# Kernel optimization log

Hardware: AMD Instinct MI355X
Metric: run time of the kernel (lower is better)

Reference implementation:

```python
import jax, jax.numpy as jnp
import numpy as np

N = 50000      # nodes
E = 800000     # edges
H = 128        # hidden_features
DEPTH = 5
G = 64         # graphs in batch
EPS = 1e-5


def _ln(x, g, b):
    m = jnp.mean(x, axis=-1, keepdims=True)
    v = jnp.mean((x - m) ** 2, axis=-1, keepdims=True)
    return (x - m) * jax.lax.rsqrt(v + EPS) * g + b


def _lin_init(key, fan_in, fan_out):
    s = 1.0 / np.sqrt(fan_in)
    kw, kb = jax.random.split(key)
    return (jax.random.uniform(kw, (fan_in, fan_out), jnp.float32, -s, s),
            jax.random.uniform(kb, (fan_out,), jnp.float32, -s, s))


def setup_inputs() -> dict:
    key = jax.random.key(0)
    ks = jax.random.split(key, 16)
    inp = {
        'x': jax.random.normal(ks[0], (N, 1), jnp.float32),
        'pos': jax.random.normal(ks[1], (N, 3), jnp.float32),
        'edge_index': jax.random.randint(ks[2], (2, E), 0, N, jnp.int32),
        'cell_offset': jax.random.normal(ks[3], (E, 3), jnp.float32),
        'unit_cell': jax.random.normal(ks[4], (3, 3), jnp.float32),
        'batch_ids': jnp.sort(jax.random.randint(ks[5], (N,), 0, G, jnp.int32)),
    }
    inp['emb_w'], inp['emb_b'] = _lin_init(ks[6], 1, H)
    # stacked per-layer params for lax.scan
    def stack(fn):
        outs = [fn(jax.random.fold_in(ks[7], i)) for i in range(DEPTH)]
        return tuple(jnp.stack(t) for t in zip(*outs))
    def layer_params(k):
        k1, k2, k3, k4 = jax.random.split(k, 4)
        mw1, mb1 = _lin_init(k1, 2 * H + 1, H)
        mw2, mb2 = _lin_init(k2, H, H)
        uw1, ub1 = _lin_init(k3, 2 * H, H)
        uw2, ub2 = _lin_init(k4, H, H)
        ones = jnp.ones((H,), jnp.float32); zeros = jnp.zeros((H,), jnp.float32)
        return (mw1, mb1, ones, zeros, mw2, mb2, ones, zeros,
                uw1, ub1, ones, zeros, uw2, ub2, ones, zeros)
    (inp['msg_w1'], inp['msg_b1'], inp['msg_g1'], inp['msg_be1'],
     inp['msg_w2'], inp['msg_b2'], inp['msg_g2'], inp['msg_be2'],
     inp['upd_w1'], inp['upd_b1'], inp['upd_g1'], inp['upd_be1'],
     inp['upd_w2'], inp['upd_b2'], inp['upd_g2'], inp['upd_be2']) = stack(layer_params)
    inp['pred_w1'], inp['pred_b1'] = _lin_init(ks[8], H, H)
    inp['pred_w2'], inp['pred_b2'] = _lin_init(ks[9], H, 1)
    return inp


def reference(x, pos, edge_index, cell_offset, unit_cell, batch_ids,
              emb_w, emb_b,
              msg_w1, msg_b1, msg_g1, msg_be1, msg_w2, msg_b2, msg_g2, msg_be2,
              upd_w1, upd_b1, upd_g1, upd_be1, upd_w2, upd_b2, upd_g2, upd_be2,
              pred_w1, pred_b1, pred_w2, pred_b2):
    src, dst = edge_index[0], edge_index[1]  # PyG: x_j = source, x_i = target
    h = x @ emb_w + emb_b  # [N, H]
    # PBC distances
    corrected = pos[dst] - cell_offset @ unit_cell  # [E, 3]
    dist = jnp.linalg.norm(corrected - pos[src], axis=-1, keepdims=True)  # [E, 1]

    def step(h, p):
        (mw1, mb1, mg1, mbe1, mw2, mb2, mg2, mbe2,
         uw1, ub1, ug1, ube1, uw2, ub2, ug2, ube2) = p
        msg = jnp.concatenate([h[dst], h[src], dist], axis=-1)  # [E, 2H+1]
        msg = jax.nn.relu(_ln(msg @ mw1 + mb1, mg1, mbe1))
        msg = jax.nn.relu(_ln(msg @ mw2 + mb2, mg2, mbe2))
        aggr = jax.ops.segment_sum(msg, dst, num_segments=N)  # scatter-add to targets
        u = jnp.concatenate([h, aggr], axis=-1)  # [N, 2H]
        u = jax.nn.relu(_ln(u @ uw1 + ub1, ug1, ube1))
        u = jax.nn.relu(_ln(u @ uw2 + ub2, ug2, ube2))
        return h + u, None  # residual

    params = (msg_w1, msg_b1, msg_g1, msg_be1, msg_w2, msg_b2, msg_g2, msg_be2,
              upd_w1, upd_b1, upd_g1, upd_be1, upd_w2, upd_b2, upd_g2, upd_be2)
    h, _ = jax.lax.scan(step, h, params)
    pooled = jax.ops.segment_sum(h, batch_ids, num_segments=G)  # global_add_pool
    return jax.nn.relu(pooled @ pred_w1 + pred_b1) @ pred_w2 + pred_b2  # [G, 1]
```

## Files before the change

### kernel.cpp

```cpp
#include <hip/hip_runtime.h>
#include <hip/hip_bf16.h>

#define NN 50000
#define NE 800000
#define HD 128
#define DEPTH 5
#define NG 64
#define LNEPS 1e-5f

typedef __attribute__((ext_vector_type(8))) short bf8;
typedef __attribute__((ext_vector_type(4))) float f4;

static __device__ __forceinline__ unsigned short bf1(float x) {
    __hip_bfloat16 b = __float2bfloat16(x);
    unsigned short r;
    __builtin_memcpy(&r, &b, 2);
    return r;
}
static __device__ __forceinline__ unsigned int cvt2(float a, float b) {
    float2 t; t.x = a; t.y = b;
    __hip_bfloat162 h = __float22bfloat162_rn(t);
    unsigned int r;
    __builtin_memcpy(&r, &h, 4);
    return r;
}


__global__ void pack_weights(const float* __restrict__ msg_w1, const float* __restrict__ msg_w2,
                             const float* __restrict__ upd_w1, const float* __restrict__ upd_w2,
                             unsigned short* __restrict__ packed) {
    const int which = blockIdx.y & 3, layer = blockIdx.y >> 2;
    const int t = blockIdx.x * 256 + threadIdx.x;
    unsigned short* lbase = packed + layer * 98304;
    if (which == 0) {
        if (t >= 32768) return;
        const int e = t & 7, l = (t >> 3) & 63, f = (t >> 9) & 15, s = t >> 13;
        const int k = s*32 + ((l >> 4) << 3) + e;
        const float* W = msg_w1 + layer*257*HD;
        const float v = (f < 8) ? W[k*HD + f*16 + (l & 15)]
                                : W[(k + 128)*HD + (f - 8)*16 + (l & 15)];
        lbase[t] = bf1(v);
        return;
    }
    const float* src; int K; unsigned short* dst;
    if (which == 1)      { src = msg_w2 + layer*HD*HD;  K = 128; dst = lbase + 32768; }
    else if (which == 2) { src = upd_w1 + layer*256*HD; K = 256; dst = lbase + 49152; }
    else                 { src = upd_w2 + layer*HD*HD;  K = 128; dst = lbase + 81920; }
    if (t >= K * HD) return;
    const int e = t & 7, l = (t >> 3) & 63, f = (t >> 9) & 7, s = t >> 12;
    const int kk = s*32 + ((l >> 4) << 3) + e;
    const int k = (which & 1) ? ((kk & 7)*16 + (kk >> 3)) : kk;
    const int n = f*16 + (l & 15);
    dst[t] = bf1(src[k*HD + n]);
}

__global__ void pack_sig(const float* __restrict__ msg_w1, const float* __restrict__ msg_g1,
                         const float* __restrict__ msg_be1, float* __restrict__ sig) {
    const int t = blockIdx.x * 256 + threadIdx.x;
    if (t >= DEPTH * 384) return;
    const int layer = t / 384, w3 = (t % 384) / 128, i = t % 128;
    const int col = (i & 7)*16 + (i >> 3);
    float v;
    if (w3 == 0)      v = msg_w1[layer*257*HD + 256*HD + col];
    else if (w3 == 1) v = msg_g1[layer*HD + col];
    else              v = msg_be1[layer*HD + col];
    sig[t] = v;
}

__global__ void embed_kernel(const float* __restrict__ x, const float* __restrict__ emb_w,
                             const float* __restrict__ emb_b,
                             float* __restrict__ h, unsigned short* __restrict__ hb) {
    const int i = blockIdx.x * 256 + threadIdx.x;
    const int n = i >> 7, j = i & 127;
    const float v = x[n] * emb_w[j] + emb_b[j];
    h[i] = v; hb[i] = bf1(v);
}

__global__ void hist_kernel(const int* __restrict__ ei, int* __restrict__ cnt) {
    const int e = blockIdx.x * 256 + threadIdx.x;
    atomicAdd(&cnt[ei[NE + e]], 1);
}

__global__ __launch_bounds__(1024) void scan_kernel(const int* __restrict__ cnt,
                                                    int* __restrict__ cur) {
    __shared__ int part[1024];
    const int t = threadIdx.x;
    const int per = 49;
    const int base = t * per;
    int s = 0;
    for (int i = 0; i < per; ++i) { const int idx = base + i; if (idx < NN) s += cnt[idx]; }
    part[t] = s; __syncthreads();
    for (int st = 1; st < 1024; st <<= 1) {
        const int v = (t >= st) ? part[t - st] : 0;
        __syncthreads();
        part[t] += v;
        __syncthreads();
    }
    int run = (t == 0) ? 0 : part[t - 1];
    for (int i = 0; i < per; ++i) {
        const int idx = base + i;
        if (idx < NN) { cur[idx] = run; run += cnt[idx]; }
    }
}

__global__ void scatter_kernel(const int* __restrict__ ei, int* __restrict__ cur,
                               int* __restrict__ sidx, int* __restrict__ ssrc,
                               int* __restrict__ sdst) {
    const int e = blockIdx.x * 256 + threadIdx.x;
    const int d = ei[NE + e];
    const int p = atomicAdd(&cur[d], 1);
    sidx[p] = e; ssrc[p] = ei[e]; sdst[p] = d;
}

__global__ void dist_kernel(const float* __restrict__ pos, const int* __restrict__ sidx,
                            const int* __restrict__ ssrc, const int* __restrict__ sdst,
                            const float* __restrict__ cell, const float* __restrict__ U,
                            float* __restrict__ dist) {
    const int p = blockIdx.x * 256 + threadIdx.x;
    const int e = sidx[p];
    const int s = ssrc[p], d = sdst[p];
    const float c0 = cell[e*3], c1 = cell[e*3+1], c2 = cell[e*3+2];
    const float ox = c0*U[0] + c1*U[3] + c2*U[6];
    const float oy = c0*U[1] + c1*U[4] + c2*U[7];
    const float oz = c0*U[2] + c1*U[5] + c2*U[8];
    const float dx = pos[d*3]   - ox - pos[s*3];
    const float dy = pos[d*3+1] - oy - pos[s*3+1];
    const float dz = pos[d*3+2] - oz - pos[s*3+2];
    dist[p] = sqrtf(dx*dx + dy*dy + dz*dz);
}

__global__ __launch_bounds__(256, 4) void y_kernel(const unsigned short* __restrict__ hb,
                         const unsigned short* __restrict__ pw,
                         const float* __restrict__ b1, unsigned short* __restrict__ y) {
    const int tid = threadIdx.x, blk = blockIdx.x;
    const int l = tid & 63, wv = tid >> 6;
    const int li = l & 15, gq = l >> 4;
    const int row = wv*16 + li;
    const int node0 = blk*64 + row;
    const int nc = (node0 < NN) ? node0 : NN - 1;
    const unsigned short* pH = hb + nc*HD + gq*8;

    f4 acc[16];
    #pragma unroll
    for (int f = 0; f < 16; ++f) { f4 z = {0.f,0.f,0.f,0.f}; acc[f] = z; }

    #pragma unroll
    for (int s = 0; s < 4; ++s) {
        const bf8 a = *(const bf8*)(pH + s*32);
        #pragma unroll
        for (int f = 0; f < 16; ++f) {
            const bf8 b = *(const bf8*)(pw + s*8192 + f*512 + l*8);
            acc[f] = __builtin_amdgcn_mfma_f32_16x16x32_bf16(a, b, acc[f], 0, 0, 0);
        }
    }

    float bv[8];
    #pragma unroll
    for (int f = 0; f < 8; ++f) bv[f] = b1[f*16 + li];

    #pragma unroll
    for (int r = 0; r < 4; ++r) {
        const int node = blk*64 + wv*16 + gq*4 + r;
        if (node < NN) {
            uint4 u;
            u.x = cvt2(acc[0][r]+bv[0], acc[1][r]+bv[1]);
            u.y = cvt2(acc[2][r]+bv[2], acc[3][r]+bv[3]);
            u.z = cvt2(acc[4][r]+bv[4], acc[5][r]+bv[5]);
            u.w = cvt2(acc[6][r]+bv[6], acc[7][r]+bv[7]);
            *(uint4*)(y + node*256 + li*8) = u;
            uint4 v;
            v.x = cvt2(acc[8][r],  acc[9][r]);
            v.y = cvt2(acc[10][r], acc[11][r]);
            v.z = cvt2(acc[12][r], acc[13][r]);
            v.w = cvt2(acc[14][r], acc[15][r]);
            *(uint4*)(y + node*256 + 128 + li*8) = v;
        }
    }
}

__global__ __launch_bounds__(128, 4) void edge_kernel(
    const unsigned short* __restrict__ y, const float* __restrict__ dist,
    const int* __restrict__ ssrc, const int* __restrict__ sdst,
    const unsigned short* __restrict__ pw2, const float* __restrict__ sig,
    const float* __restrict__ b2, const float* __restrict__ g2,
    const float* __restrict__ be2, float* __restrict__ aggr)
{
    __shared__ unsigned short lds[64 * 128];
    __shared__ int dstl[64];
    char* ldsb = (char*)lds;
    const int tid = threadIdx.x, blk = blockIdx.x;
    const int l = tid & 63, wv = tid >> 6;
    const int li = l & 15, gq = l >> 4;

    if (tid < 64) dstl[tid] = sdst[blk*64 + tid];

    {
        const int rl = l >> 1, half = l & 1;
        const int row = wv*32 + rl;
        const int e = blk*64 + row;
        const int dn = sdst[e], sn = ssrc[e];
        const float dv = dist[e];
        const unsigned short* pd = y + dn*256 + half*64;
        const unsigned short* pS = y + sn*256 + 128 + half*64;
        const float* wl = sig + half*64;

        float msum[64];
        #pragma unroll
        for (int c = 0; c < 8; ++c) {
            const uint4 ud = *(const uint4*)(pd + c*8);
            const uint4 us = *(const uint4*)(pS + c*8);
            const float4 wa = *(const float4*)(wl + c*8);
            const float4 wb = *(const float4*)(wl + c*8 + 4);
            const unsigned int du[4] = {ud.x, ud.y, ud.z, ud.w};
            const unsigned int su[4] = {us.x, us.y, us.z, us.w};
            const float ww[8] = {wa.x,wa.y,wa.z,wa.w, wb.x,wb.y,wb.z,wb.w};
            #pragma unroll
            for (int k = 0; k < 4; ++k) {
                const float d0 = __uint_as_float(du[k] << 16);
                const float d1 = __uint_as_float(du[k] & 0xffff0000u);
                const float s0 = __uint_as_float(su[k] << 16);
                const float s1 = __uint_as_float(su[k] & 0xffff0000u);
                msum[c*8 + 2*k]     = d0 + s0 + dv*ww[2*k];
                msum[c*8 + 2*k + 1] = d1 + s1 + dv*ww[2*k+1];
            }
        }
        float s1 = 0.f, s2 = 0.f;
        #pragma unroll
        for (int i = 0; i < 64; ++i) { s1 += msum[i]; s2 += msum[i]*msum[i]; }
        s1 += __shfl_xor(s1, 1);
        s2 += __shfl_xor(s2, 1);
        const float mean = s1 * (1.f/HD);
        const float rstd = rsqrtf(s2*(1.f/HD) - mean*mean + LNEPS);

        const float* g1p = sig + 128 + half*64;
        const float* e1p = sig + 256 + half*64;
        const int rsw = (row & 15) << 4;
        const int base = row*256 + half*128;
        #pragma unroll
        for (int c = 0; c < 8; ++c) {
            const float4 ga = *(const float4*)(g1p + c*8);
            const float4 gb = *(const float4*)(g1p + c*8 + 4);
            const float4 ea = *(const float4*)(e1p + c*8);
            const float4 eb = *(const float4*)(e1p + c*8 + 4);
            const float gg[8] = {ga.x,ga.y,ga.z,ga.w, gb.x,gb.y,gb.z,gb.w};
            const float ee[8] = {ea.x,ea.y,ea.z,ea.w, eb.x,eb.y,eb.z,eb.w};
            float t[8];
            #pragma unroll
            for (int k = 0; k < 8; ++k)
                t[k] = fmaxf((msum[c*8+k] - mean)*rstd*gg[k] + ee[k], 0.f);
            uint4 u;
            u.x = cvt2(t[0], t[1]); u.y = cvt2(t[2], t[3]);
            u.z = cvt2(t[4], t[5]); u.w = cvt2(t[6], t[7]);
            *(uint4*)(ldsb + ((base + c*16) ^ rsw)) = u;
        }
    }

    f4 acc2[2][8];
    #pragma unroll
    for (int m = 0; m < 2; ++m)
        #pragma unroll
        for (int f = 0; f < 8; ++f) { f4 z = {0.f,0.f,0.f,0.f}; acc2[m][f] = z; }
    #pragma unroll
    for (int s = 0; s < 4; ++s) {
        bf8 breg[8];
        #pragma unroll
        for (int f = 0; f < 8; ++f) breg[f] = *(const bf8*)(pw2 + s*4096 + f*512 + l*8);
        #pragma unroll
        for (int m = 0; m < 2; ++m) {
            const int ar = wv*32 + m*16 + li;
            const bf8 a = *(const bf8*)(ldsb + ((ar*256 + s*64 + gq*16) ^ ((ar & 15) << 4)));
            #pragma unroll
            for (int f = 0; f < 8; ++f)
                acc2[m][f] = __builtin_amdgcn_mfma_f32_16x16x32_bf16(a, breg[f], acc2[m][f], 0, 0, 0);
        }
    }

    {
        float bb2[8], gg2[8], be2v[8];
        #pragma unroll
        for (int f = 0; f < 8; ++f) {
            const int n = f*16 + li;
            bb2[f] = b2[n]; gg2[f] = g2[n]; be2v[f] = be2[n];
        }
        #pragma unroll
        for (int m = 0; m < 2; ++m) {
            float ps[4] = {0,0,0,0}, pq[4] = {0,0,0,0};
            #pragma unroll
            for (int f = 0; f < 8; ++f)
                #pragma unroll
                for (int r = 0; r < 4; ++r) {
                    const float v = acc2[m][f][r] + bb2[f];
                    acc2[m][f][r] = v;
                    ps[r] += v; pq[r] += v*v;
                }
            #pragma unroll
            for (int mm = 1; mm < 16; mm <<= 1)
                #pragma unroll
                for (int r = 0; r < 4; ++r) {
                    ps[r] += __shfl_xor(ps[r], mm);
                    pq[r] += __shfl_xor(pq[r], mm);
                }
            #pragma unroll
            for (int r = 0; r < 4; ++r) {
                const float mean = ps[r] * (1.f/HD);
                const float rstd = rsqrtf(pq[r]*(1.f/HD) - mean*mean + LNEPS);
                const int row = wv*32 + m*16 + gq*4 + r;
                float vv[8];
                #pragma unroll
                for (int f = 0; f < 8; ++f)
                    vv[f] = fmaxf((acc2[m][f][r] - mean)*rstd*gg2[f] + be2v[f], 0.f);
                uint4 u;
                u.x = cvt2(vv[0], vv[1]); u.y = cvt2(vv[2], vv[3]);
                u.z = cvt2(vv[4], vv[5]); u.w = cvt2(vv[6], vv[7]);
                *(uint4*)(ldsb + ((row*256 + li*16) ^ ((row & 15) << 4))) = u;
            }
        }
    }
    __syncthreads();

    {
        const int jp = tid & 63, hh = tid >> 6;
        const int j0 = jp*2, j1 = j0 + 1;
        const int jj0 = (j0 & 7)*16 + (j0 >> 3);
        const int jj1 = (j1 & 7)*16 + (j1 >> 3);
        const int r0 = hh * 32;
        int curd = dstl[r0];
        float a0 = 0.f, a1 = 0.f;
        #pragma unroll 4
        for (int i = 0; i < 32; ++i) {
            const int row = r0 + i;
            const int d = dstl[row];
            const unsigned int u = *(const unsigned int*)(ldsb + ((row*256 + jp*4) ^ ((row & 15) << 4)));
            if (d != curd) {
                unsafeAtomicAdd(&aggr[curd*HD + jj0], a0);
                unsafeAtomicAdd(&aggr[curd*HD + jj1], a1);
                a0 = a1 = 0.f; curd = d;
            }
            a0 += __uint_as_float(u << 16);
            a1 += __uint_as_float(u & 0xffff0000u);
        }
        unsafeAtomicAdd(&aggr[curd*HD + jj0], a0);
        unsafeAtomicAdd(&aggr[curd*HD + jj1], a1);
    }
}

__global__ __launch_bounds__(256, 4) void node_kernel(
    unsigned short* __restrict__ hb, float* __restrict__ aggr,
    const unsigned short* __restrict__ pw,
    const float* __restrict__ b1, const float* __restrict__ g1, const float* __restrict__ be1,
    const float* __restrict__ b2, const float* __restrict__ g2, const float* __restrict__ be2,
    float* __restrict__ h)
{
    __shared__ unsigned short lds[64 * 128];
    char* ldsb = (char*)lds;
    const int tid = threadIdx.x, blk = blockIdx.x;
    const int l = tid & 63, wv = tid >> 6;
    const int li = l & 15, gq = l >> 4;

    const int row = wv*16 + li;
    const int nA = blk*64 + row;
    const int nc = (nA < NN) ? nA : NN - 1;
    const unsigned short* pH = hb + nc*HD + gq*8;
    float* pA = aggr + nc*HD + gq*8;

    f4 acc[8];
    #pragma unroll
    for (int f = 0; f < 8; ++f) { f4 z = {0.f,0.f,0.f,0.f}; acc[f] = z; }

    #pragma unroll
    for (int s = 0; s < 8; ++s) {
        bf8 breg[8];
        #pragma unroll
        for (int f = 0; f < 8; ++f) breg[f] = *(const bf8*)(pw + s*4096 + f*512 + l*8);
        bf8 a;
        if (s < 4) {
            a = *(const bf8*)(pH + s*32);
        } else {
            const float4 a0 = *(const float4*)(pA + (s-4)*32);
            const float4 a1 = *(const float4*)(pA + (s-4)*32 + 4);
            union { unsigned int u[4]; bf8 v; } pk;
            pk.u[0] = cvt2(a0.x, a0.y); pk.u[1] = cvt2(a0.z, a0.w);
            pk.u[2] = cvt2(a1.x, a1.y); pk.u[3] = cvt2(a1.z, a1.w);
            a = pk.v;
        }
        #pragma unroll
        for (int f = 0; f < 8; ++f)
            acc[f] = __builtin_amdgcn_mfma_f32_16x16x32_bf16(a, breg[f], acc[f], 0, 0, 0);
    }

    {
        const float4 z = {0.f,0.f,0.f,0.f};
        if (nA < NN) {
            #pragma unroll
            for (int s = 0; s < 4; ++s) { *(float4*)(pA + s*32) = z; *(float4*)(pA + s*32 + 4) = z; }
        }
    }

    {
        float bb[8], gg[8], be[8];
        #pragma unroll
        for (int f = 0; f < 8; ++f) {
            const int n = f*16 + li;
            bb[f] = b1[n]; gg[f] = g1[n]; be[f] = be1[n];
        }
        float ps[4] = {0,0,0,0}, pq[4] = {0,0,0,0};
        #pragma unroll
        for (int f = 0; f < 8; ++f)
            #pragma unroll
            for (int r = 0; r < 4; ++r) {
                const float v = acc[f][r] + bb[f];
                acc[f][r] = v;
                ps[r] += v; pq[r] += v*v;
            }
        #pragma unroll
        for (int mm = 1; mm < 16; mm <<= 1)
            #pragma unroll
            for (int r = 0; r < 4; ++r) {
                ps[r] += __shfl_xor(ps[r], mm);
                pq[r] += __shfl_xor(pq[r], mm);
            }
        #pragma unroll
        for (int r = 0; r < 4; ++r) {
            const float mean = ps[r] * (1.f/HD);
            const float rstd = rsqrtf(pq[r]*(1.f/HD) - mean*mean + LNEPS);
            const int rw = wv*16 + gq*4 + r;
            float vv[8];
            #pragma unroll
            for (int f = 0; f < 8; ++f)
                vv[f] = fmaxf((acc[f][r] - mean)*rstd*gg[f] + be[f], 0.f);
            uint4 u;
            u.x = cvt2(vv[0], vv[1]); u.y = cvt2(vv[2], vv[3]);
            u.z = cvt2(vv[4], vv[5]); u.w = cvt2(vv[6], vv[7]);
            *(uint4*)(ldsb + ((rw*256 + li*16) ^ ((rw & 15) << 4))) = u;
        }
    }

    const unsigned short* pw2 = pw + 32768;
    f4 acc2[8];
    #pragma unroll
    for (int f = 0; f < 8; ++f) { f4 z = {0.f,0.f,0.f,0.f}; acc2[f] = z; }
    #pragma unroll
    for (int s = 0; s < 4; ++s) {
        bf8 breg[8];
        #pragma unroll
        for (int f = 0; f < 8; ++f) breg[f] = *(const bf8*)(pw2 + s*4096 + f*512 + l*8);
        const int ar = wv*16 + li;
        const bf8 a = *(const bf8*)(ldsb + ((ar*256 + s*64 + gq*16) ^ ((ar & 15) << 4)));
        #pragma unroll
        for (int f = 0; f < 8; ++f)
            acc2[f] = __builtin_amdgcn_mfma_f32_16x16x32_bf16(a, breg[f], acc2[f], 0, 0, 0);
    }

    {
        float bb2[8], gg2[8], be2v[8];
        #pragma unroll
        for (int f = 0; f < 8; ++f) {
            const int n = f*16 + li;
            bb2[f] = b2[n]; gg2[f] = g2[n]; be2v[f] = be2[n];
        }
        float ps[4] = {0,0,0,0}, pq[4] = {0,0,0,0};
        #pragma unroll
        for (int f = 0; f < 8; ++f)
            #pragma unroll
            for (int r = 0; r < 4; ++r) {
                const float v = acc2[f][r] + bb2[f];
                acc2[f][r] = v;
                ps[r] += v; pq[r] += v*v;
            }
        #pragma unroll
        for (int mm = 1; mm < 16; mm <<= 1)
            #pragma unroll
            for (int r = 0; r < 4; ++r) {
                ps[r] += __shfl_xor(ps[r], mm);
                pq[r] += __shfl_xor(pq[r], mm);
            }
        #pragma unroll
        for (int r = 0; r < 4; ++r) {
            const int node = blk*64 + wv*16 + gq*4 + r;
            if (node < NN) {
                const float mean = ps[r] * (1.f/HD);
                const float rstd = rsqrtf(pq[r]*(1.f/HD) - mean*mean + LNEPS);
                #pragma unroll
                for (int f = 0; f < 8; ++f) {
                    const int n = f*16 + li;
                    float v = (acc2[f][r] - mean)*rstd*gg2[f] + be2v[f];
                    v = fmaxf(v, 0.f);
                    const int idx = node*HD + n;
                    const float nh = h[idx] + v;
                    h[idx] = nh;
                    hb[idx] = bf1(nh);
                }
            }
        }
    }
}

__global__ void pool_kernel(const float* __restrict__ h, const int* __restrict__ bids,
                            float* __restrict__ pooled) {
    const int j = threadIdx.x;
    const int n0 = blockIdx.x * 256;
    if (n0 >= NN) return;
    int cur = bids[n0];
    float acc = 0.f;
    for (int i = 0; i < 256; ++i) {
        const int n = n0 + i;
        if (n >= NN) break;
        const int b = bids[n];
        if (b != cur) { unsafeAtomicAdd(&pooled[cur*HD + j], acc); acc = 0.f; cur = b; }
        acc += h[n*HD + j];
    }
    unsafeAtomicAdd(&pooled[cur*HD + j], acc);
}

__global__ void pred_kernel(const float* __restrict__ pooled, const float* __restrict__ w1,
                            const float* __restrict__ pb1, const float* __restrict__ w2,
                            const float* __restrict__ pb2, float* __restrict__ out) {
    const int g = blockIdx.x, j = threadIdx.x;
    __shared__ float pg[128];
    __shared__ float red[128];
    pg[j] = pooled[g*HD + j];
    __syncthreads();
    float z = pb1[j];
    for (int k = 0; k < 128; ++k) z += pg[k] * w1[k*HD + j];
    red[j] = fmaxf(z, 0.f) * w2[j];
    __syncthreads();
    for (int st = 64; st > 0; st >>= 1) {
        if (j < st) red[j] += red[j + st];
        __syncthreads();
    }
    if (j == 0) out[g] = red[0] + pb2[0];
}

extern "C" void kernel_launch(void* const* d_in, const int* in_sizes, int n_in,
                              void* d_out, int out_size, void* d_ws, size_t ws_size,
                              hipStream_t stream) {
    const float* x       = (const float*)d_in[0];
    const float* pos     = (const float*)d_in[1];
    const int*   ei      = (const int*)  d_in[2];
    const float* cell    = (const float*)d_in[3];
    const float* U       = (const float*)d_in[4];
    const int*   bids    = (const int*)  d_in[5];
    const float* emb_w   = (const float*)d_in[6];
    const float* emb_b   = (const float*)d_in[7];
    const float* msg_w1  = (const float*)d_in[8];
    const float* msg_b1  = (const float*)d_in[9];
    const float* msg_g1  = (const float*)d_in[10];
    const float* msg_be1 = (const float*)d_in[11];
    const float* msg_w2  = (const float*)d_in[12];
    const float* msg_b2  = (const float*)d_in[13];
    const float* msg_g2  = (const float*)d_in[14];
    const float* msg_be2 = (const float*)d_in[15];
    const float* upd_w1  = (const float*)d_in[16];
    const float* upd_b1  = (const float*)d_in[17];
    const float* upd_g1  = (const float*)d_in[18];
    const float* upd_be1 = (const float*)d_in[19];
    const float* upd_w2  = (const float*)d_in[20];
    const float* upd_b2  = (const float*)d_in[21];
    const float* upd_g2  = (const float*)d_in[22];
    const float* upd_be2 = (const float*)d_in[23];
    const float* pred_w1 = (const float*)d_in[24];
    const float* pred_b1 = (const float*)d_in[25];
    const float* pred_w2 = (const float*)d_in[26];
    const float* pred_b2 = (const float*)d_in[27];

    char* ws = (char*)d_ws;
    float*          h      = (float*)          ws;
    unsigned short* hb     = (unsigned short*)(ws + 25600000);
    float*          aggr   = (float*)         (ws + 38400000);
    float*          dist   = (float*)         (ws + 64000000);
    float*          pooled = (float*)         (ws + 67200000);
    unsigned short* packed = (unsigned short*)(ws + 67232768);
    int*            cnt    = (int*)           (ws + 68215808);
    int*            cur    = (int*)           (ws + 68416512);
    int*            sidx   = (int*)           (ws + 68617216);
    int*            ssrc   = (int*)           (ws + 71817216);
    int*            sdst   = (int*)           (ws + 75017216);
    float*          sig    = (float*)         (ws + 78217216);
    unsigned short* y      = (unsigned short*)(ws + 78224896);

    hipMemsetAsync(aggr, 0, (size_t)NN * HD * sizeof(float), stream);
    hipMemsetAsync(pooled, 0, (size_t)NG * HD * sizeof(float), stream);
    hipMemsetAsync(cnt, 0, (size_t)NN * sizeof(int), stream);

    dim3 pgrid(128, DEPTH * 4);
    pack_weights<<<pgrid, 256, 0, stream>>>(msg_w1, msg_w2, upd_w1, upd_w2, packed);
    pack_sig<<<(DEPTH*384 + 255)/256, 256, 0, stream>>>(msg_w1, msg_g1, msg_be1, sig);
    embed_kernel<<<(NN * HD) / 256, 256, 0, stream>>>(x, emb_w, emb_b, h, hb);

    hist_kernel<<<NE / 256, 256, 0, stream>>>(ei, cnt);
    scan_kernel<<<1, 1024, 0, stream>>>(cnt, cur);
    scatter_kernel<<<NE / 256, 256, 0, stream>>>(ei, cur, sidx, ssrc, sdst);
    dist_kernel<<<NE / 256, 256, 0, stream>>>(pos, sidx, ssrc, sdst, cell, U, dist);

    for (int layer = 0; layer < DEPTH; ++layer) {
        const unsigned short* pl = packed + layer * 98304;
        y_kernel<<<(NN + 63) / 64, 256, 0, stream>>>(hb, pl, msg_b1 + layer*HD, y);
        edge_kernel<<<NE / 64, 128, 0, stream>>>(
            y, dist, ssrc, sdst, pl + 32768, sig + layer*384,
            msg_b2 + layer*HD, msg_g2 + layer*HD, msg_be2 + layer*HD,
            aggr);
        node_kernel<<<(NN + 63) / 64, 256, 0, stream>>>(
            hb, aggr, pl + 49152,
            upd_b1 + layer*HD, upd_g1 + layer*HD, upd_be1 + layer*HD,
            upd_b2 + layer*HD, upd_g2 + layer*HD, upd_be2 + layer*HD,
            h);
    }

    pool_kernel<<<(NN + 255) / 256, 128, 0, stream>>>(h, bids, pooled);
    pred_kernel<<<NG, 128, 0, stream>>>(pooled, pred_w1, pred_b1, pred_w2, pred_b2, (float*)d_out);
}
```

Before: 1.509 ms.

## Fuse per-node message projection into node kernel and precompute layer-0 projection

Removes the separate y_kernel. The next layer's per-node projection of h through msg_w1 now runs inside node_kernel, reusing the freshly updated h staged in LDS. Layer 0's projection is computed analytically from the embedding, since y is linear in x, via a small precompute kernel plus the embed kernel. The edge kernel's scatter and LDS swizzle are also reworked to one column per thread over 64 rows, with an 8-row swizzle and a matching permutation in the weight packing. This saves a launch and a global re-read of hb per layer, at the cost of higher register and LDS pressure in node_kernel.

New measurement: 1.336 ms. 1.13x faster.

```diff
diff --git a/kernel.cpp b/kernel.cpp
--- a/kernel.cpp
+++ b/kernel.cpp
@@ -35,7 +35,8 @@
     if (which == 0) {
         if (t >= 32768) return;
         const int e = t & 7, l = (t >> 3) & 63, f = (t >> 9) & 15, s = t >> 13;
-        const int k = s*32 + ((l >> 4) << 3) + e;
+        const int kk = s*32 + ((l >> 4) << 3) + e;
+        const int k = (kk & 7)*16 + (kk >> 3);
         const float* W = msg_w1 + layer*257*HD;
         const float v = (f < 8) ? W[k*HD + f*16 + (l & 15)]
                                 : W[(k + 128)*HD + (f - 8)*16 + (l & 15)];
@@ -67,13 +68,35 @@
     sig[t] = v;
 }
 
+__global__ void pack_y0(const float* __restrict__ emb_w, const float* __restrict__ emb_b,
+                        const float* __restrict__ msg_w1, const float* __restrict__ msg_b1,
+                        float* __restrict__ y0ab) {
+    const int t = threadIdx.x;
+    const int half = t >> 7, c = t & 127;
+    const float* W = msg_w1 + half*128*HD;
+    float a = 0.f, b = 0.f;
+    for (int k = 0; k < 128; ++k) {
+        const float w = W[k*HD + c];
+        a += emb_w[k] * w;
+        b += emb_b[k] * w;
+    }
+    if (half == 0) b += msg_b1[c];
+    const int i = half*128 + ((c & 15)*8 + (c >> 4));
+    y0ab[i] = a; y0ab[256 + i] = b;
+}
+
 __global__ void embed_kernel(const float* __restrict__ x, const float* __restrict__ emb_w,
-                             const float* __restrict__ emb_b,
-                             float* __restrict__ h, unsigned short* __restrict__ hb) {
+                             const float* __restrict__ emb_b, const float* __restrict__ y0ab,
+                             float* __restrict__ h, unsigned short* __restrict__ hb,
+                             unsigned short* __restrict__ y) {
     const int i = blockIdx.x * 256 + threadIdx.x;
-    const int n = i >> 7, j = i & 127;
-    const float v = x[n] * emb_w[j] + emb_b[j];
-    h[i] = v; hb[i] = bf1(v);
+    const int n = i >> 8, t = i & 255;
+    const float xv = x[n];
+    y[i] = bf1(xv * y0ab[t] + y0ab[256 + t]);
+    if (t < 128) {
+        const float v = xv * emb_w[t] + emb_b[t];
+        h[n*HD + t] = v; hb[n*HD + t] = bf1(v);
+    }
 }
 
 __global__ void hist_kernel(const int* __restrict__ ei, int* __restrict__ cnt) {
@@ -129,55 +152,6 @@
     dist[p] = sqrtf(dx*dx + dy*dy + dz*dz);
 }
 
-__global__ __launch_bounds__(256, 4) void y_kernel(const unsigned short* __restrict__ hb,
-                         const unsigned short* __restrict__ pw,
-                         const float* __restrict__ b1, unsigned short* __restrict__ y) {
-    const int tid = threadIdx.x, blk = blockIdx.x;
-    const int l = tid & 63, wv = tid >> 6;
-    const int li = l & 15, gq = l >> 4;
-    const int row = wv*16 + li;
-    const int node0 = blk*64 + row;
-    const int nc = (node0 < NN) ? node0 : NN - 1;
-    const unsigned short* pH = hb + nc*HD + gq*8;
-
-    f4 acc[16];
-    #pragma unroll
-    for (int f = 0; f < 16; ++f) { f4 z = {0.f,0.f,0.f,0.f}; acc[f] = z; }
-
-    #pragma unroll
-    for (int s = 0; s < 4; ++s) {
-        const bf8 a = *(const bf8*)(pH + s*32);
-        #pragma unroll
-        for (int f = 0; f < 16; ++f) {
-            const bf8 b = *(const bf8*)(pw + s*8192 + f*512 + l*8);
-            acc[f] = __builtin_amdgcn_mfma_f32_16x16x32_bf16(a, b, acc[f], 0, 0, 0);
-        }
-    }
-
-    float bv[8];
-    #pragma unroll
-    for (int f = 0; f < 8; ++f) bv[f] = b1[f*16 + li];
-
-    #pragma unroll
-    for (int r = 0; r < 4; ++r) {
-        const int node = blk*64 + wv*16 + gq*4 + r;
-        if (node < NN) {
-            uint4 u;
-            u.x = cvt2(acc[0][r]+bv[0], acc[1][r]+bv[1]);
-            u.y = cvt2(acc[2][r]+bv[2], acc[3][r]+bv[3]);
-            u.z = cvt2(acc[4][r]+bv[4], acc[5][r]+bv[5]);
-            u.w = cvt2(acc[6][r]+bv[6], acc[7][r]+bv[7]);
-            *(uint4*)(y + node*256 + li*8) = u;
-            uint4 v;
-            v.x = cvt2(acc[8][r],  acc[9][r]);
-            v.y = cvt2(acc[10][r], acc[11][r]);
-            v.z = cvt2(acc[12][r], acc[13][r]);
-            v.w = cvt2(acc[14][r], acc[15][r]);
-            *(uint4*)(y + node*256 + 128 + li*8) = v;
-        }
-    }
-}
-
 __global__ __launch_bounds__(128, 4) void edge_kernel(
     const unsigned short* __restrict__ y, const float* __restrict__ dist,
     const int* __restrict__ ssrc, const int* __restrict__ sdst,
@@ -234,7 +208,7 @@
 
         const float* g1p = sig + 128 + half*64;
         const float* e1p = sig + 256 + half*64;
-        const int rsw = (row & 15) << 4;
+        const int rsw = (row & 7) << 4;
         const int base = row*256 + half*128;
         #pragma unroll
         for (int c = 0; c < 8; ++c) {
@@ -268,7 +242,7 @@
         #pragma unroll
         for (int m = 0; m < 2; ++m) {
             const int ar = wv*32 + m*16 + li;
-            const bf8 a = *(const bf8*)(ldsb + ((ar*256 + s*64 + gq*16) ^ ((ar & 15) << 4)));
+            const bf8 a = *(const bf8*)(ldsb + ((ar*256 + s*64 + gq*16) ^ ((ar & 7) << 4)));
             #pragma unroll
             for (int f = 0; f < 8; ++f)
                 acc2[m][f] = __builtin_amdgcn_mfma_f32_16x16x32_bf16(a, breg[f], acc2[m][f], 0, 0, 0);
@@ -312,35 +286,26 @@
                 uint4 u;
                 u.x = cvt2(vv[0], vv[1]); u.y = cvt2(vv[2], vv[3]);
                 u.z = cvt2(vv[4], vv[5]); u.w = cvt2(vv[6], vv[7]);
-                *(uint4*)(ldsb + ((row*256 + li*16) ^ ((row & 15) << 4))) = u;
+                *(uint4*)(ldsb + ((row*256 + li*16) ^ ((row & 7) << 4))) = u;
             }
         }
     }
     __syncthreads();
 
     {
-        const int jp = tid & 63, hh = tid >> 6;
-        const int j0 = jp*2, j1 = j0 + 1;
-        const int jj0 = (j0 & 7)*16 + (j0 >> 3);
-        const int jj1 = (j1 & 7)*16 + (j1 >> 3);
-        const int r0 = hh * 32;
-        int curd = dstl[r0];
-        float a0 = 0.f, a1 = 0.f;
+        const int j = tid;
+        const int jj = (j & 7)*16 + (j >> 3);
+        int curd = dstl[0];
+        float a0 = 0.f;
         #pragma unroll 4
-        for (int i = 0; i < 32; ++i) {
-            const int row = r0 + i;
+        for (int row = 0; row < 64; ++row) {
             const int d = dstl[row];
-            const unsigned int u = *(const unsigned int*)(ldsb + ((row*256 + jp*4) ^ ((row & 15) << 4)));
-            if (d != curd) {
-                unsafeAtomicAdd(&aggr[curd*HD + jj0], a0);
-                unsafeAtomicAdd(&aggr[curd*HD + jj1], a1);
-                a0 = a1 = 0.f; curd = d;
-            }
-            a0 += __uint_as_float(u << 16);
-            a1 += __uint_as_float(u & 0xffff0000u);
-        }
-        unsafeAtomicAdd(&aggr[curd*HD + jj0], a0);
-        unsafeAtomicAdd(&aggr[curd*HD + jj1], a1);
+            const unsigned short u = *(const unsigned short*)(ldsb + ((row*256 + j*2) ^ ((row & 7) << 4)));
+            const float v = __uint_as_float(((unsigned int)u) << 16);
+            if (d != curd) { unsafeAtomicAdd(&aggr[curd*HD + jj], a0); a0 = 0.f; curd = d; }
+            a0 += v;
+        }
+        unsafeAtomicAdd(&aggr[curd*HD + jj], a0);
     }
 }
 
@@ -349,7 +314,9 @@
     const unsigned short* __restrict__ pw,
     const float* __restrict__ b1, const float* __restrict__ g1, const float* __restrict__ be1,
     const float* __restrict__ b2, const float* __restrict__ g2, const float* __restrict__ be2,
-    float* __restrict__ h)
+    float* __restrict__ h,
+    const unsigned short* __restrict__ pwy, const float* __restrict__ b1y,
+    unsigned short* __restrict__ y, int do_y)
 {
     __shared__ unsigned short lds[64 * 128];
     char* ldsb = (char*)lds;
@@ -477,19 +444,69 @@
         #pragma unroll
         for (int r = 0; r < 4; ++r) {
             const int node = blk*64 + wv*16 + gq*4 + r;
+            const float mean = ps[r] * (1.f/HD);
+            const float rstd = rsqrtf(pq[r]*(1.f/HD) - mean*mean + LNEPS);
+            const int rw = wv*16 + gq*4 + r;
+            float nhv[8];
             if (node < NN) {
-                const float mean = ps[r] * (1.f/HD);
-                const float rstd = rsqrtf(pq[r]*(1.f/HD) - mean*mean + LNEPS);
                 #pragma unroll
                 for (int f = 0; f < 8; ++f) {
                     const int n = f*16 + li;
-                    float v = (acc2[f][r] - mean)*rstd*gg2[f] + be2v[f];
-                    v = fmaxf(v, 0.f);
+                    float v = fmaxf((acc2[f][r] - mean)*rstd*gg2[f] + be2v[f], 0.f);
                     const int idx = node*HD + n;
                     const float nh = h[idx] + v;
-                    h[idx] = nh;
-                    hb[idx] = bf1(nh);
+                    h[idx] = nh; hb[idx] = bf1(nh);
+                    nhv[f] = nh;
                 }
+            } else {
+                #pragma unroll
+                for (int f = 0; f < 8; ++f) nhv[f] = 0.f;
+            }
+            uint4 u;
+            u.x = cvt2(nhv[0], nhv[1]); u.y = cvt2(nhv[2], nhv[3]);
+            u.z = cvt2(nhv[4], nhv[5]); u.w = cvt2(nhv[6], nhv[7]);
+            *(uint4*)(ldsb + ((rw*256 + li*16) ^ ((rw & 15) << 4))) = u;
+        }
+    }
+
+    if (do_y) {
+        f4 accy[16];
+        #pragma unroll
+        for (int f = 0; f < 16; ++f) { f4 z = {0.f,0.f,0.f,0.f}; accy[f] = z; }
+        #pragma unroll
+        for (int s = 0; s < 4; ++s) {
+            const int ar = wv*16 + li;
+            const bf8 a = *(const bf8*)(ldsb + ((ar*256 + s*64 + gq*16) ^ ((ar & 15) << 4)));
+            #pragma unroll
+            for (int fh = 0; fh < 2; ++fh) {
+                bf8 breg[8];
+                #pragma unroll
+                for (int f = 0; f < 8; ++f)
+                    breg[f] = *(const bf8*)(pwy + s*8192 + (fh*8 + f)*512 + l*8);
+                #pragma unroll
+                for (int f = 0; f < 8; ++f)
+                    accy[fh*8 + f] = __builtin_amdgcn_mfma_f32_16x16x32_bf16(a, breg[f], accy[fh*8 + f], 0, 0, 0);
+            }
+        }
+        float bv[8];
+        #pragma unroll
+        for (int f = 0; f < 8; ++f) bv[f] = b1y[f*16 + li];
+        #pragma unroll
+        for (int r = 0; r < 4; ++r) {
+            const int node = blk*64 + wv*16 + gq*4 + r;
+            if (node < NN) {
+                uint4 u;
+                u.x = cvt2(accy[0][r]+bv[0], accy[1][r]+bv[1]);
+                u.y = cvt2(accy[2][r]+bv[2], accy[3][r]+bv[3]);
+                u.z = cvt2(accy[4][r]+bv[4], accy[5][r]+bv[5]);
+                u.w = cvt2(accy[6][r]+bv[6], accy[7][r]+bv[7]);
+                *(uint4*)(y + node*256 + li*8) = u;
+                uint4 v;
+                v.x = cvt2(accy[8][r],  accy[9][r]);
+                v.y = cvt2(accy[10][r], accy[11][r]);
+                v.z = cvt2(accy[12][r], accy[13][r]);
+                v.w = cvt2(accy[14][r], accy[15][r]);
+                *(uint4*)(y + node*256 + 128 + li*8) = v;
             }
         }
     }
@@ -576,7 +593,8 @@
     int*            ssrc   = (int*)           (ws + 71817216);
     int*            sdst   = (int*)           (ws + 75017216);
     float*          sig    = (float*)         (ws + 78217216);
-    unsigned short* y      = (unsigned short*)(ws + 78224896);
+    float*          y0ab   = (float*)         (ws + 78224896);
+    unsigned short* y      = (unsigned short*)(ws + 78226944);
 
     hipMemsetAsync(aggr, 0, (size_t)NN * HD * sizeof(float), stream);
     hipMemsetAsync(pooled, 0, (size_t)NG * HD * sizeof(float), stream);
@@ -585,7 +603,8 @@
     dim3 pgrid(128, DEPTH * 4);
     pack_weights<<<pgrid, 256, 0, stream>>>(msg_w1, msg_w2, upd_w1, upd_w2, packed);
     pack_sig<<<(DEPTH*384 + 255)/256, 256, 0, stream>>>(msg_w1, msg_g1, msg_be1, sig);
-    embed_kernel<<<(NN * HD) / 256, 256, 0, stream>>>(x, emb_w, emb_b, h, hb);
+    pack_y0<<<1, 256, 0, stream>>>(emb_w, emb_b, msg_w1, msg_b1, y0ab);
+    embed_kernel<<<NN, 256, 0, stream>>>(x, emb_w, emb_b, y0ab, h, hb, y);
 
     hist_kernel<<<NE / 256, 256, 0, stream>>>(ei, cnt);
     scan_kernel<<<1, 1024, 0, stream>>>(cnt, cur);
@@ -594,16 +613,18 @@
 
     for (int layer = 0; layer < DEPTH; ++layer) {
         const unsigned short* pl = packed + layer * 98304;
-        y_kernel<<<(NN + 63) / 64, 256, 0, stream>>>(hb, pl, msg_b1 + layer*HD, y);
         edge_kernel<<<NE / 64, 128, 0, stream>>>(
             y, dist, ssrc, sdst, pl + 32768, sig + layer*384,
             msg_b2 + layer*HD, msg_g2 + layer*HD, msg_be2 + layer*HD,
             aggr);
+        const int do_y = (layer + 1 < DEPTH) ? 1 : 0;
+        const int nl = do_y ? layer + 1 : layer;
         node_kernel<<<(NN + 63) / 64, 256, 0, stream>>>(
             hb, aggr, pl + 49152,
             upd_b1 + layer*HD, upd_g1 + layer*HD, upd_be1 + layer*HD,
             upd_b2 + layer*HD, upd_g2 + layer*HD, upd_be2 + layer*HD,
-            h);
+            h,
+            packed + nl * 98304, msg_b1 + nl*HD, y, do_y);
     }
 
     pool_kernel<<<(NN + 255) / 256, 128, 0, stream>>>(h, bids, pooled);
```
